# Performance work log

Measured on AMD Instinct MI355X. Metric: run time of the kernel, lower is better.

## Reference

```python
import jax, jax.numpy as jnp
import numpy as np

H = 56; W = 56; WS = 7; SHIFT = 3; HEADS = 4; DIM = 128
N = WS * WS  # 49 tokens per window
EPS = 1e-5


def _rel_pos_index():
    c = np.stack(np.meshgrid(np.arange(WS), np.arange(WS), indexing='ij')).reshape(2, -1)
    r = (c[:, :, None] - c[:, None, :]).transpose(1, 2, 0)
    r[..., 0] += WS - 1
    r[..., 1] += WS - 1
    r[..., 0] *= 2 * WS - 1
    return jnp.asarray(r.sum(-1))  # [N, N] int


def _attn_mask():
    img = np.zeros((H, W))
    sl = (slice(0, -WS), slice(-WS, -SHIFT), slice(-SHIFT, None))
    cnt = 0
    for hs in sl:
        for ws_ in sl:
            img[hs, ws_] = cnt
            cnt += 1
    mw = img.reshape(H // WS, WS, W // WS, WS).transpose(0, 2, 1, 3).reshape(-1, N)
    d = mw[:, None, :] - mw[:, :, None]  # [nW, N, N]
    return jnp.asarray(np.where(d != 0, -100.0, 0.0).astype(np.float32))


def _ln(x, w, b):
    m = x.mean(-1, keepdims=True)
    v = ((x - m) ** 2).mean(-1, keepdims=True)
    return (x - m) / jnp.sqrt(v + EPS) * w + b


def setup_inputs() -> dict:
    key = jax.random.key(0)
    ks = jax.random.split(key, 8)
    B = 64
    return {
        'x': jax.random.normal(ks[0], (B, H * W, DIM), jnp.float32),
        'qkv_w': jax.random.normal(ks[1], (DIM, 3 * DIM), jnp.float32) * 0.02,
        'qkv_b': jnp.zeros((3 * DIM,), jnp.float32),
        'proj_w': jax.random.normal(ks[2], (DIM, DIM), jnp.float32) * 0.02,
        'proj_b': jnp.zeros((DIM,), jnp.float32),
        'rpb_table': jax.random.normal(ks[3], ((2 * WS - 1) ** 2, HEADS), jnp.float32) * 0.02,
        'norm1_w': jnp.ones((DIM,), jnp.float32),
        'norm1_b': jnp.zeros((DIM,), jnp.float32),
        'norm2_w': jnp.ones((DIM,), jnp.float32),
        'norm2_b': jnp.zeros((DIM,), jnp.float32),
        'mlp_w1': jax.random.normal(ks[4], (DIM, 4 * DIM), jnp.float32) * 0.02,
        'mlp_b1': jnp.zeros((4 * DIM,), jnp.float32),
        'mlp_w2': jax.random.normal(ks[5], (4 * DIM, DIM), jnp.float32) * 0.02,
        'mlp_b2': jnp.zeros((DIM,), jnp.float32),
    }


def reference(x, qkv_w, qkv_b, proj_w, proj_b, rpb_table,
              norm1_w, norm1_b, norm2_w, norm2_b,
              mlp_w1, mlp_b1, mlp_w2, mlp_b2):
    B = x.shape[0]
    C = DIM
    hd = C // HEADS
    shortcut = x
    h = _ln(x, norm1_w, norm1_b).reshape(B, H, W, C)
    # cyclic shift
    h = jnp.roll(h, (-SHIFT, -SHIFT), axis=(1, 2))
    # window partition -> [B*nW, N, C]
    xw = h.reshape(B, H // WS, WS, W // WS, WS, C).transpose(0, 1, 3, 2, 4, 5).reshape(-1, N, C)
    qkv = (xw @ qkv_w + qkv_b).reshape(-1, N, 3, HEADS, hd).transpose(2, 0, 3, 1, 4)
    q, k, v = qkv[0] * (hd ** -0.5), qkv[1], qkv[2]  # [B*nW, heads, N, hd]
    attn = jnp.einsum('whnd,whmd->whnm', q, k)
    bias = rpb_table[_rel_pos_index().reshape(-1)].reshape(N, N, HEADS).transpose(2, 0, 1)
    attn = attn + bias[None]
    mask = _attn_mask()  # [nW, N, N]
    nW = mask.shape[0]
    attn = attn.reshape(B, nW, HEADS, N, N) + mask[None, :, None]
    attn = jax.nn.softmax(attn.reshape(-1, HEADS, N, N), axis=-1)
    out = jnp.einsum('whnm,whmd->wnhd', attn, v).reshape(-1, N, C)
    out = out @ proj_w + proj_b
    # window reverse + reverse shift
    out = out.reshape(B, H // WS, W // WS, WS, WS, C).transpose(0, 1, 3, 2, 4, 5).reshape(B, H, W, C)
    out = jnp.roll(out, (SHIFT, SHIFT), axis=(1, 2)).reshape(B, H * W, C)
    x = shortcut + out
    h2 = _ln(x, norm2_w, norm2_b)
    h2 = jax.nn.gelu(h2 @ mlp_w1 + mlp_b1, approximate=False) @ mlp_w2 + mlp_b2
    return x + h2
```

## Files before the change

### kernel.cpp

```cpp
#include <hip/hip_runtime.h>

#define HH 56
#define WW2 56
#define WS 7
#define SHIFT 3
#define HEADS 4
#define DIM 128
#define NTOK 49
#define BATCH 64
#define TOKENS (BATCH*HH*WW2)
#define NWIN 64
#define WINDOWS (BATCH*NWIN)

typedef __bf16 bf16x8 __attribute__((ext_vector_type(8)));
typedef float  f32x4  __attribute__((ext_vector_type(4)));

__device__ __forceinline__ unsigned short f2bf(float f) {
  unsigned u = __float_as_uint(f);
  u += 0x7fffu + ((u >> 16) & 1u);
  return (unsigned short)(u >> 16);
}

__device__ __forceinline__ void st4(unsigned short* p, float a, float b, float c, float d) {
  ushort4 pk; pk.x = f2bf(a); pk.y = f2bf(b); pk.z = f2bf(c); pk.w = f2bf(d);
  *(ushort4*)p = pk;
}

__device__ __forceinline__ int reg3(int g) { return g >= 53 ? 2 : (g >= 49 ? 1 : 0); }

__global__ __launch_bounds__(256) void k_prep(
    const float* __restrict__ qkv_w, const float* __restrict__ proj_w,
    const float* __restrict__ w1, const float* __restrict__ w2,
    unsigned short* __restrict__ qkvwT, unsigned short* __restrict__ projwT,
    unsigned short* __restrict__ w1T, unsigned short* __restrict__ w2T)
{
  int idx = blockIdx.x * 256 + threadIdx.x;
  if (idx < 49152) {
    int n = idx >> 7, k = idx & 127;
    qkvwT[idx] = f2bf(qkv_w[k * 384 + n]);
  } else if (idx < 65536) {
    int i = idx - 49152; int n = i >> 7, k = i & 127;
    projwT[i] = f2bf(proj_w[k * 128 + n]);
  } else if (idx < 131072) {
    int i = idx - 65536; int n = i >> 7, k = i & 127;
    w1T[i] = f2bf(w1[k * 512 + n]);
  } else {
    int i = idx - 131072; int n = i >> 9, k = i & 511;
    w2T[i] = f2bf(w2[k * 128 + n]);
  }
}

__global__ __launch_bounds__(256) void k_tbl(const float* __restrict__ rpb, float* __restrict__ tbl)
{
  int idx = blockIdx.x * 256 + threadIdx.x;
  int kt = idx & 63, qt = (idx >> 6) & 63, h = (idx >> 12) & 3, cls = idx >> 14;
  float v;
  if (qt >= NTOK || kt >= NTOK) v = -3e38f;
  else {
    int qi = qt / 7, qj = qt % 7, ki = kt / 7, kj = kt % 7;
    int bi = (cls & 2) ? 49 : 0, bj = (cls & 1) ? 49 : 0;
    int rq = reg3(bi + qi) * 3 + reg3(bj + qj);
    int rk = reg3(bi + ki) * 3 + reg3(bj + kj);
    v = rpb[((qi - ki + 6) * 13 + (qj - kj + 6)) * HEADS + h] + (rq != rk ? -100.0f : 0.0f);
  }
  tbl[idx] = v;
}

__global__ __launch_bounds__(256) void k_ln1_window(
    const float* __restrict__ x, const float* __restrict__ w,
    const float* __restrict__ b, unsigned short* __restrict__ xw)
{
  int lane = threadIdx.x & 63;
  int t = blockIdx.x * 4 + (threadIdx.x >> 6);
  const float* xp = x + (size_t)t * DIM;
  float2 v = *(const float2*)(xp + lane * 2);
  float s = v.x + v.y;
  float sq = v.x * v.x + v.y * v.y;
  #pragma unroll
  for (int off = 32; off; off >>= 1) {
    s += __shfl_xor(s, off);
    sq += __shfl_xor(sq, off);
  }
  float mean = s * (1.0f / DIM);
  float var = sq * (1.0f / DIM) - mean * mean;
  float rs = rsqrtf(var + 1e-5f);
  float2 wv = *(const float2*)(w + lane * 2);
  float2 bv = *(const float2*)(b + lane * 2);
  float y0 = (v.x - mean) * rs * wv.x + bv.x;
  float y1 = (v.y - mean) * rs * wv.y + bv.y;
  int bi = t / (HH * WW2);
  int r = t % (HH * WW2);
  int i = r / WW2, j = r % WW2;
  int si = i >= SHIFT ? i - SHIFT : i + (HH - SHIFT);
  int sj = j >= SHIFT ? j - SHIFT : j + (WW2 - SHIFT);
  int win = bi * NWIN + (si / WS) * 8 + (sj / WS);
  int tok = (si % WS) * WS + (sj % WS);
  unsigned pack = ((unsigned)f2bf(y1) << 16) | (unsigned)f2bf(y0);
  *(unsigned*)(xw + ((size_t)(win * NTOK + tok)) * DIM + lane * 2) = pack;
}

__global__ __launch_bounds__(256, 2) void k_attn(
    const unsigned short* __restrict__ xw,
    const unsigned short* __restrict__ qkvwT,
    const float* __restrict__ qkv_b,
    const unsigned short* __restrict__ projwT,
    const float* __restrict__ proj_b,
    const float* __restrict__ tbl,
    unsigned short* __restrict__ attn_out)
{
  __shared__ __align__(16) unsigned short s_x[64 * 136];
  __shared__ __align__(16) unsigned short s_qk[64 * 264];
  __shared__ __align__(16) unsigned short s_vT[128 * 72];

  int tid = threadIdx.x;
  int wave = tid >> 6;
  int lane = tid & 63;
  int l = lane & 15, g = lane >> 4;
  int win = blockIdx.x;
  int wi = (win & 63) >> 3, wj = win & 7;

  const unsigned short* xwin = xw + (size_t)win * (NTOK * DIM);
  for (int idx = tid; idx < NTOK * 16; idx += 256) {
    int row = idx >> 4, seg = idx & 15;
    *(uint4*)&s_x[row * 136 + seg * 8] = *(const uint4*)(xwin + row * DIM + seg * 8);
  }
  for (int idx = tid; idx < 15 * 17; idx += 256) {
    int row = 49 + idx / 17, seg = idx % 17;
    *(uint4*)&s_x[row * 136 + seg * 8] = make_uint4(0, 0, 0, 0);
  }
  __syncthreads();

  bf16x8 xf[4][4];
  #pragma unroll
  for (int nt = 0; nt < 4; ++nt)
    #pragma unroll
    for (int kk = 0; kk < 4; ++kk)
      xf[nt][kk] = *(const bf16x8*)&s_x[(nt * 16 + l) * 136 + kk * 32 + g * 8];

  #pragma unroll
  for (int wti = 0; wti < 6; ++wti) {
    int wt = wave * 6 + wti;
    bf16x8 wf[4];
    #pragma unroll
    for (int kk = 0; kk < 4; ++kk)
      wf[kk] = *(const bf16x8*)(qkvwT + (size_t)(wt * 16 + l) * DIM + kk * 32 + g * 8);
    f32x4 acc[4];
    #pragma unroll
    for (int nt = 0; nt < 4; ++nt) acc[nt] = (f32x4){0.f, 0.f, 0.f, 0.f};
    #pragma unroll
    for (int kk = 0; kk < 4; ++kk)
      #pragma unroll
      for (int nt = 0; nt < 4; ++nt)
        acc[nt] = __builtin_amdgcn_mfma_f32_16x16x32_bf16(wf[kk], xf[nt][kk], acc[nt], 0, 0, 0);
    float4 b4 = *(const float4*)(qkv_b + wt * 16 + g * 4);
    if (wt < 16) {
      float sc = wt < 8 ? 0.17677669529663687f : 1.0f;
      #pragma unroll
      for (int nt = 0; nt < 4; ++nt)
        st4(&s_qk[(nt * 16 + l) * 264 + wt * 16 + g * 4],
            (acc[nt][0] + b4.x) * sc, (acc[nt][1] + b4.y) * sc,
            (acc[nt][2] + b4.z) * sc, (acc[nt][3] + b4.w) * sc);
    } else {
      int d0 = wt * 16 - 256 + g * 4;
      #pragma unroll
      for (int nt = 0; nt < 4; ++nt) {
        s_vT[(d0 + 0) * 72 + nt * 16 + l] = f2bf(acc[nt][0] + b4.x);
        s_vT[(d0 + 1) * 72 + nt * 16 + l] = f2bf(acc[nt][1] + b4.y);
        s_vT[(d0 + 2) * 72 + nt * 16 + l] = f2bf(acc[nt][2] + b4.z);
        s_vT[(d0 + 3) * 72 + nt * 16 + l] = f2bf(acc[nt][3] + b4.w);
      }
    }
  }
  __syncthreads();

  int h = wave;
  bf16x8 kf[4], qf[4];
  #pragma unroll
  for (int mt = 0; mt < 4; ++mt)
    kf[mt] = *(const bf16x8*)&s_qk[(mt * 16 + l) * 264 + 128 + h * 32 + g * 8];
  #pragma unroll
  for (int nt = 0; nt < 4; ++nt)
    qf[nt] = *(const bf16x8*)&s_qk[(nt * 16 + l) * 264 + h * 32 + g * 8];
  __syncthreads();

  int clsid = ((wi == 7) ? 2 : 0) | ((wj == 7) ? 1 : 0);
  const float* tb = tbl + ((clsid * 4 + h) << 12);
  f32x4 sc[4][4];
  #pragma unroll
  for (int nt = 0; nt < 4; ++nt)
    #pragma unroll
    for (int mt = 0; mt < 4; ++mt) {
      f32x4 ci = *(const f32x4*)(tb + (nt * 16 + l) * 64 + mt * 16 + g * 4);
      sc[mt][nt] = __builtin_amdgcn_mfma_f32_16x16x32_bf16(kf[mt], qf[nt], ci, 0, 0, 0);
    }

  #pragma unroll
  for (int nt = 0; nt < 4; ++nt) {
    float m = sc[0][nt][0];
    #pragma unroll
    for (int mt = 0; mt < 4; ++mt)
      #pragma unroll
      for (int rr = 0; rr < 4; ++rr) m = fmaxf(m, sc[mt][nt][rr]);
    m = fmaxf(m, __shfl_xor(m, 16));
    m = fmaxf(m, __shfl_xor(m, 32));
    float ssum = 0.f;
    #pragma unroll
    for (int mt = 0; mt < 4; ++mt)
      #pragma unroll
      for (int rr = 0; rr < 4; ++rr) {
        float e = __expf(sc[mt][nt][rr] - m);
        sc[mt][nt][rr] = e;
        ssum += e;
      }
    ssum += __shfl_xor(ssum, 16);
    ssum += __shfl_xor(ssum, 32);
    float inv = 1.0f / ssum;
    #pragma unroll
    for (int mt = 0; mt < 4; ++mt)
      st4(&s_qk[(nt * 16 + l) * 264 + h * 64 + mt * 16 + g * 4],
          sc[mt][nt][0] * inv, sc[mt][nt][1] * inv, sc[mt][nt][2] * inv, sc[mt][nt][3] * inv);
  }

  bf16x8 vf[2][2], pf[4][2];
  #pragma unroll
  for (int dt = 0; dt < 2; ++dt)
    #pragma unroll
    for (int kk = 0; kk < 2; ++kk)
      vf[dt][kk] = *(const bf16x8*)&s_vT[(h * 32 + dt * 16 + l) * 72 + kk * 32 + g * 8];
  #pragma unroll
  for (int nt = 0; nt < 4; ++nt)
    #pragma unroll
    for (int kk = 0; kk < 2; ++kk)
      pf[nt][kk] = *(const bf16x8*)&s_qk[(nt * 16 + l) * 264 + h * 64 + kk * 32 + g * 8];
  #pragma unroll
  for (int dt = 0; dt < 2; ++dt)
    #pragma unroll
    for (int nt = 0; nt < 4; ++nt) {
      f32x4 a = (f32x4){0.f, 0.f, 0.f, 0.f};
      a = __builtin_amdgcn_mfma_f32_16x16x32_bf16(vf[dt][0], pf[nt][0], a, 0, 0, 0);
      a = __builtin_amdgcn_mfma_f32_16x16x32_bf16(vf[dt][1], pf[nt][1], a, 0, 0, 0);
      st4(&s_x[(nt * 16 + l) * 136 + h * 32 + dt * 16 + g * 4], a[0], a[1], a[2], a[3]);
    }
  __syncthreads();

  unsigned short* stage = s_vT;
  bf16x8 of[4][4];
  #pragma unroll
  for (int nt = 0; nt < 4; ++nt)
    #pragma unroll
    for (int kk = 0; kk < 4; ++kk)
      of[nt][kk] = *(const bf16x8*)&s_x[(nt * 16 + l) * 136 + kk * 32 + g * 8];
  #pragma unroll
  for (int wti = 0; wti < 2; ++wti) {
    int wt = wave * 2 + wti;
    bf16x8 wf[4];
    #pragma unroll
    for (int kk = 0; kk < 4; ++kk)
      wf[kk] = *(const bf16x8*)(projwT + (size_t)(wt * 16 + l) * DIM + kk * 32 + g * 8);
    f32x4 acc[4];
    #pragma unroll
    for (int nt = 0; nt < 4; ++nt) acc[nt] = (f32x4){0.f, 0.f, 0.f, 0.f};
    #pragma unroll
    for (int kk = 0; kk < 4; ++kk)
      #pragma unroll
      for (int nt = 0; nt < 4; ++nt)
        acc[nt] = __builtin_amdgcn_mfma_f32_16x16x32_bf16(wf[kk], of[nt][kk], acc[nt], 0, 0, 0);
    float4 b4 = *(const float4*)(proj_b + wt * 16 + g * 4);
    #pragma unroll
    for (int nt = 0; nt < 4; ++nt)
      st4(&stage[(nt * 16 + l) * 136 + wt * 16 + g * 4],
          acc[nt][0] + b4.x, acc[nt][1] + b4.y, acc[nt][2] + b4.z, acc[nt][3] + b4.w);
  }
  __syncthreads();

  unsigned short* outp = attn_out + (size_t)win * (NTOK * DIM);
  for (int idx = tid; idx < NTOK * 16; idx += 256) {
    int row = idx >> 4, seg = idx & 15;
    *(uint4*)(outp + idx * 8) = *(const uint4*)&stage[row * 136 + seg * 8];
  }
}

__device__ __forceinline__ float gelu_f(float x) {
  float x2 = x * x;
  float t = x * __builtin_fmaf(x2, -0.10294429f, -2.3022077f);
  float e = __builtin_amdgcn_exp2f(t);
  return x * __builtin_amdgcn_rcpf(1.0f + e);
}

__global__ __launch_bounds__(256) void k_mlp(
    const float* __restrict__ x, const unsigned short* __restrict__ attn,
    const float* __restrict__ n2w, const float* __restrict__ n2b,
    const unsigned short* __restrict__ w1T, const float* __restrict__ b1,
    const unsigned short* __restrict__ w2T, const float* __restrict__ b2,
    float* __restrict__ io)
{
  __shared__ __align__(16) unsigned short s_t[2][64 * 136];
  __shared__ float s_part[64][4][2];
  int tid = threadIdx.x;
  int wave = tid >> 6;
  int lane = tid & 63;
  int l = lane & 15, g = lane >> 4;
  size_t m0 = (size_t)blockIdx.x * 64;
  int col0 = wave * 32 + g * 4;

  float4 xz[4][2];
  float sA[4], sQ[4];
  #pragma unroll
  for (int nt = 0; nt < 4; ++nt) {
    int row = nt * 16 + l;
    int t = (int)m0 + row;
    int bi = t / (HH * WW2);
    int r = t % (HH * WW2);
    int i = r / WW2, j = r % WW2;
    int si = i >= SHIFT ? i - SHIFT : i + (HH - SHIFT);
    int sj = j >= SHIFT ? j - SHIFT : j + (WW2 - SHIFT);
    int win = bi * NWIN + (si / WS) * 8 + (sj / WS);
    int tok = (si % WS) * WS + (sj % WS);
    const float* xp = x + (size_t)t * DIM;
    const unsigned short* ap = attn + ((size_t)(win * NTOK + tok)) * DIM;
    float s = 0.f, sq = 0.f;
    #pragma unroll
    for (int wti = 0; wti < 2; ++wti) {
      int col = col0 + wti * 16;
      float4 xv = *(const float4*)(xp + col);
      ushort4 av = *(const ushort4*)(ap + col);
      float4 z;
      z.x = xv.x + __uint_as_float((unsigned)av.x << 16);
      z.y = xv.y + __uint_as_float((unsigned)av.y << 16);
      z.z = xv.z + __uint_as_float((unsigned)av.z << 16);
      z.w = xv.w + __uint_as_float((unsigned)av.w << 16);
      xz[nt][wti] = z;
      s += z.x + z.y + z.z + z.w;
      sq += z.x * z.x + z.y * z.y + z.z * z.z + z.w * z.w;
      *(float4*)(io + (size_t)t * DIM + col) = z;
    }
    s += __shfl_xor(s, 16); s += __shfl_xor(s, 32);
    sq += __shfl_xor(sq, 16); sq += __shfl_xor(sq, 32);
    sA[nt] = s; sQ[nt] = sq;
  }
  if (g == 0) {
    #pragma unroll
    for (int nt = 0; nt < 4; ++nt) {
      s_part[nt * 16 + l][wave][0] = sA[nt];
      s_part[nt * 16 + l][wave][1] = sQ[nt];
    }
  }
  __syncthreads();
  float4 wv0 = *(const float4*)(n2w + col0);
  float4 wv1 = *(const float4*)(n2w + col0 + 16);
  float4 bv0 = *(const float4*)(n2b + col0);
  float4 bv1 = *(const float4*)(n2b + col0 + 16);
  #pragma unroll
  for (int nt = 0; nt < 4; ++nt) {
    int row = nt * 16 + l;
    float s = 0.f, sq = 0.f;
    #pragma unroll
    for (int wv = 0; wv < 4; ++wv) { s += s_part[row][wv][0]; sq += s_part[row][wv][1]; }
    float mean = s * (1.0f / DIM);
    float var = sq * (1.0f / DIM) - mean * mean;
    float rs = rsqrtf(var + 1e-5f);
    float4 z0 = xz[nt][0], z1 = xz[nt][1];
    st4(&s_t[1][row * 136 + col0],
        (z0.x - mean) * rs * wv0.x + bv0.x, (z0.y - mean) * rs * wv0.y + bv0.y,
        (z0.z - mean) * rs * wv0.z + bv0.z, (z0.w - mean) * rs * wv0.w + bv0.w);
    st4(&s_t[1][row * 136 + col0 + 16],
        (z1.x - mean) * rs * wv1.x + bv1.x, (z1.y - mean) * rs * wv1.y + bv1.y,
        (z1.z - mean) * rs * wv1.z + bv1.z, (z1.w - mean) * rs * wv1.w + bv1.w);
  }
  __syncthreads();

  bf16x8 hf[4][4];
  #pragma unroll
  for (int nt = 0; nt < 4; ++nt)
    #pragma unroll
    for (int kk = 0; kk < 4; ++kk)
      hf[nt][kk] = *(const bf16x8*)&s_t[1][(nt * 16 + l) * 136 + kk * 32 + g * 8];

  f32x4 o[2][4];
  #pragma unroll
  for (int wti = 0; wti < 2; ++wti)
    #pragma unroll
    for (int nt = 0; nt < 4; ++nt) o[wti][nt] = (f32x4){0.f, 0.f, 0.f, 0.f};

  for (int c = 0; c < 4; ++c) {
    unsigned short* buf = s_t[c & 1];
    #pragma unroll
    for (int wti = 0; wti < 2; ++wti) {
      int wt = wave * 2 + wti;
      int n0 = c * 128 + wt * 16;
      bf16x8 wf[4];
      #pragma unroll
      for (int kk = 0; kk < 4; ++kk)
        wf[kk] = *(const bf16x8*)(w1T + (size_t)(n0 + l) * DIM + kk * 32 + g * 8);
      f32x4 acc[4];
      #pragma unroll
      for (int nt = 0; nt < 4; ++nt) acc[nt] = (f32x4){0.f, 0.f, 0.f, 0.f};
      #pragma unroll
      for (int kk = 0; kk < 4; ++kk)
        #pragma unroll
        for (int nt = 0; nt < 4; ++nt)
          acc[nt] = __builtin_amdgcn_mfma_f32_16x16x32_bf16(wf[kk], hf[nt][kk], acc[nt], 0, 0, 0);
      float4 b4 = *(const float4*)(b1 + n0 + g * 4);
      #pragma unroll
      for (int nt = 0; nt < 4; ++nt)
        st4(&buf[(nt * 16 + l) * 136 + wt * 16 + g * 4],
            gelu_f(acc[nt][0] + b4.x), gelu_f(acc[nt][1] + b4.y),
            gelu_f(acc[nt][2] + b4.z), gelu_f(acc[nt][3] + b4.w));
    }
    __syncthreads();
    #pragma unroll
    for (int kk = 0; kk < 4; ++kk) {
      bf16x8 tf[4];
      #pragma unroll
      for (int nt = 0; nt < 4; ++nt)
        tf[nt] = *(const bf16x8*)&buf[(nt * 16 + l) * 136 + kk * 32 + g * 8];
      #pragma unroll
      for (int wti = 0; wti < 2; ++wti) {
        int wt = wave * 2 + wti;
        bf16x8 wf2 = *(const bf16x8*)(w2T + (size_t)(wt * 16 + l) * 512 + c * 128 + kk * 32 + g * 8);
        #pragma unroll
        for (int nt = 0; nt < 4; ++nt)
          o[wti][nt] = __builtin_amdgcn_mfma_f32_16x16x32_bf16(wf2, tf[nt], o[wti][nt], 0, 0, 0);
      }
    }
  }

  #pragma unroll
  for (int wti = 0; wti < 2; ++wti) {
    int wt = wave * 2 + wti;
    float4 b4 = *(const float4*)(b2 + wt * 16 + g * 4);
    #pragma unroll
    for (int nt = 0; nt < 4; ++nt) {
      float* p = io + (m0 + nt * 16 + l) * DIM + wt * 16 + g * 4;
      float4 pv = *(float4*)p;
      pv.x += o[wti][nt][0] + b4.x;
      pv.y += o[wti][nt][1] + b4.y;
      pv.z += o[wti][nt][2] + b4.z;
      pv.w += o[wti][nt][3] + b4.w;
      *(float4*)p = pv;
    }
  }
}

extern "C" void kernel_launch(void* const* d_in, const int* in_sizes, int n_in,
                              void* d_out, int out_size, void* d_ws, size_t ws_size,
                              hipStream_t stream) {
  const float* x       = (const float*)d_in[0];
  const float* qkv_w   = (const float*)d_in[1];
  const float* qkv_b   = (const float*)d_in[2];
  const float* proj_w  = (const float*)d_in[3];
  const float* proj_b  = (const float*)d_in[4];
  const float* rpb     = (const float*)d_in[5];
  const float* n1w     = (const float*)d_in[6];
  const float* n1b     = (const float*)d_in[7];
  const float* n2w     = (const float*)d_in[8];
  const float* n2b     = (const float*)d_in[9];
  const float* mlp_w1  = (const float*)d_in[10];
  const float* mlp_b1  = (const float*)d_in[11];
  const float* mlp_w2  = (const float*)d_in[12];
  const float* mlp_b2  = (const float*)d_in[13];
  float* out = (float*)d_out;

  char* ws = (char*)d_ws;
  const size_t TOKB = (size_t)TOKENS * DIM * 2;
  unsigned short* xw     = (unsigned short*)(ws);
  unsigned short* attn_o = (unsigned short*)(ws + TOKB);
  unsigned short* qkvwT  = (unsigned short*)(ws + 2 * TOKB);
  unsigned short* projwT = (unsigned short*)(ws + 2 * TOKB + 98304);
  unsigned short* w1T    = (unsigned short*)(ws + 2 * TOKB + 98304 + 32768);
  unsigned short* w2T    = (unsigned short*)(ws + 2 * TOKB + 98304 + 32768 + 131072);
  float*          tbl    = (float*)(ws + 2 * TOKB + 98304 + 32768 + 131072 + 131072);

  k_prep<<<768, 256, 0, stream>>>(qkv_w, proj_w, mlp_w1, mlp_w2, qkvwT, projwT, w1T, w2T);
  k_tbl<<<256, 256, 0, stream>>>(rpb, tbl);
  k_ln1_window<<<TOKENS / 4, 256, 0, stream>>>(x, n1w, n1b, xw);
  k_attn<<<WINDOWS, 256, 0, stream>>>(xw, qkvwT, qkv_b, projwT, proj_b, tbl, attn_o);
  k_mlp<<<TOKENS / 64, 256, 0, stream>>>(x, attn_o, n2w, n2b, w1T, mlp_b1, w2T, mlp_b2, out);
}
```

Baseline: 500.2 us.

## Fuse LN1 and window partition into attention kernel; keep residual in registers

Removes the separate LN1/window-partition kernel: each attention block now gathers its shifted window rows directly from x in fp32, normalizes them and writes bf16 into shared memory. This removes a bf16 intermediate round trip through global memory and one launch. In the MLP kernel, the first residual sum is kept in registers and combined with the MLP output in a single store, instead of being written and then read back. The cost is more registers in the attention kernel, which holds 13 row pairs per lane, and strided gathers from x.

Result: faster. 465.9 us (-6.9%).

```diff
diff --git a/kernel.cpp b/kernel.cpp
--- a/kernel.cpp
+++ b/kernel.cpp
@@ -66,41 +66,9 @@
   tbl[idx] = v;
 }
 
-__global__ __launch_bounds__(256) void k_ln1_window(
-    const float* __restrict__ x, const float* __restrict__ w,
-    const float* __restrict__ b, unsigned short* __restrict__ xw)
-{
-  int lane = threadIdx.x & 63;
-  int t = blockIdx.x * 4 + (threadIdx.x >> 6);
-  const float* xp = x + (size_t)t * DIM;
-  float2 v = *(const float2*)(xp + lane * 2);
-  float s = v.x + v.y;
-  float sq = v.x * v.x + v.y * v.y;
-  #pragma unroll
-  for (int off = 32; off; off >>= 1) {
-    s += __shfl_xor(s, off);
-    sq += __shfl_xor(sq, off);
-  }
-  float mean = s * (1.0f / DIM);
-  float var = sq * (1.0f / DIM) - mean * mean;
-  float rs = rsqrtf(var + 1e-5f);
-  float2 wv = *(const float2*)(w + lane * 2);
-  float2 bv = *(const float2*)(b + lane * 2);
-  float y0 = (v.x - mean) * rs * wv.x + bv.x;
-  float y1 = (v.y - mean) * rs * wv.y + bv.y;
-  int bi = t / (HH * WW2);
-  int r = t % (HH * WW2);
-  int i = r / WW2, j = r % WW2;
-  int si = i >= SHIFT ? i - SHIFT : i + (HH - SHIFT);
-  int sj = j >= SHIFT ? j - SHIFT : j + (WW2 - SHIFT);
-  int win = bi * NWIN + (si / WS) * 8 + (sj / WS);
-  int tok = (si % WS) * WS + (sj % WS);
-  unsigned pack = ((unsigned)f2bf(y1) << 16) | (unsigned)f2bf(y0);
-  *(unsigned*)(xw + ((size_t)(win * NTOK + tok)) * DIM + lane * 2) = pack;
-}
-
 __global__ __launch_bounds__(256, 2) void k_attn(
-    const unsigned short* __restrict__ xw,
+    const float* __restrict__ x,
+    const float* __restrict__ n1w, const float* __restrict__ n1b,
     const unsigned short* __restrict__ qkvwT,
     const float* __restrict__ qkv_b,
     const unsigned short* __restrict__ projwT,
@@ -118,11 +86,43 @@
   int l = lane & 15, g = lane >> 4;
   int win = blockIdx.x;
   int wi = (win & 63) >> 3, wj = win & 7;
-
-  const unsigned short* xwin = xw + (size_t)win * (NTOK * DIM);
-  for (int idx = tid; idx < NTOK * 16; idx += 256) {
-    int row = idx >> 4, seg = idx & 15;
-    *(uint4*)&s_x[row * 136 + seg * 8] = *(const uint4*)(xwin + row * DIM + seg * 8);
+  int bi = win >> 6;
+
+  {
+    float2 wv1 = *(const float2*)(n1w + lane * 2);
+    float2 bv1 = *(const float2*)(n1b + lane * 2);
+    float2 vr[13];
+    #pragma unroll
+    for (int rr = 0; rr < 13; ++rr) {
+      int row = wave + rr * 4;
+      if (row < NTOK) {
+        int ti = row / 7, tj = row % 7;
+        int i = wi * WS + ti + SHIFT; if (i >= HH) i -= HH;
+        int j = wj * WS + tj + SHIFT; if (j >= WW2) j -= WW2;
+        const float* xp = x + ((size_t)(bi * (HH * WW2) + i * WW2 + j)) * DIM;
+        vr[rr] = *(const float2*)(xp + lane * 2);
+      }
+    }
+    #pragma unroll
+    for (int rr = 0; rr < 13; ++rr) {
+      int row = wave + rr * 4;
+      if (row < NTOK) {
+        float2 v = vr[rr];
+        float s = v.x + v.y, sq = v.x * v.x + v.y * v.y;
+        #pragma unroll
+        for (int off = 32; off; off >>= 1) {
+          s += __shfl_xor(s, off);
+          sq += __shfl_xor(sq, off);
+        }
+        float mean = s * (1.0f / DIM);
+        float var = sq * (1.0f / DIM) - mean * mean;
+        float rs = rsqrtf(var + 1e-5f);
+        float y0 = (v.x - mean) * rs * wv1.x + bv1.x;
+        float y1 = (v.y - mean) * rs * wv1.y + bv1.y;
+        unsigned pack = ((unsigned)f2bf(y1) << 16) | (unsigned)f2bf(y0);
+        *(unsigned*)&s_x[row * 136 + lane * 2] = pack;
+      }
+    }
   }
   for (int idx = tid; idx < 15 * 17; idx += 256) {
     int row = 49 + idx / 17, seg = idx % 17;
@@ -332,7 +332,6 @@
       xz[nt][wti] = z;
       s += z.x + z.y + z.z + z.w;
       sq += z.x * z.x + z.y * z.y + z.z * z.z + z.w * z.w;
-      *(float4*)(io + (size_t)t * DIM + col) = z;
     }
     s += __shfl_xor(s, 16); s += __shfl_xor(s, 32);
     sq += __shfl_xor(sq, 16); sq += __shfl_xor(sq, 32);
@@ -431,13 +430,13 @@
     float4 b4 = *(const float4*)(b2 + wt * 16 + g * 4);
     #pragma unroll
     for (int nt = 0; nt < 4; ++nt) {
-      float* p = io + (m0 + nt * 16 + l) * DIM + wt * 16 + g * 4;
-      float4 pv = *(float4*)p;
-      pv.x += o[wti][nt][0] + b4.x;
-      pv.y += o[wti][nt][1] + b4.y;
-      pv.z += o[wti][nt][2] + b4.z;
-      pv.w += o[wti][nt][3] + b4.w;
-      *(float4*)p = pv;
+      float4 z = xz[nt][wti];
+      float4 pv;
+      pv.x = z.x + o[wti][nt][0] + b4.x;
+      pv.y = z.y + o[wti][nt][1] + b4.y;
+      pv.z = z.z + o[wti][nt][2] + b4.z;
+      pv.w = z.w + o[wti][nt][3] + b4.w;
+      *(float4*)(io + (m0 + nt * 16 + l) * DIM + wt * 16 + g * 4) = pv;
     }
   }
 }
@@ -463,17 +462,15 @@
 
   char* ws = (char*)d_ws;
   const size_t TOKB = (size_t)TOKENS * DIM * 2;
-  unsigned short* xw     = (unsigned short*)(ws);
-  unsigned short* attn_o = (unsigned short*)(ws + TOKB);
-  unsigned short* qkvwT  = (unsigned short*)(ws + 2 * TOKB);
-  unsigned short* projwT = (unsigned short*)(ws + 2 * TOKB + 98304);
-  unsigned short* w1T    = (unsigned short*)(ws + 2 * TOKB + 98304 + 32768);
-  unsigned short* w2T    = (unsigned short*)(ws + 2 * TOKB + 98304 + 32768 + 131072);
-  float*          tbl    = (float*)(ws + 2 * TOKB + 98304 + 32768 + 131072 + 131072);
+  unsigned short* attn_o = (unsigned short*)(ws);
+  unsigned short* qkvwT  = (unsigned short*)(ws + TOKB);
+  unsigned short* projwT = (unsigned short*)(ws + TOKB + 98304);
+  unsigned short* w1T    = (unsigned short*)(ws + TOKB + 98304 + 32768);
+  unsigned short* w2T    = (unsigned short*)(ws + TOKB + 98304 + 32768 + 131072);
+  float*          tbl    = (float*)(ws + TOKB + 98304 + 32768 + 131072 + 131072);
 
   k_prep<<<768, 256, 0, stream>>>(qkv_w, proj_w, mlp_w1, mlp_w2, qkvwT, projwT, w1T, w2T);
   k_tbl<<<256, 256, 0, stream>>>(rpb, tbl);
-  k_ln1_window<<<TOKENS / 4, 256, 0, stream>>>(x, n1w, n1b, xw);
-  k_attn<<<WINDOWS, 256, 0, stream>>>(xw, qkvwT, qkv_b, projwT, proj_b, tbl, attn_o);
+  k_attn<<<WINDOWS, 256, 0, stream>>>(x, n1w, n1b, qkvwT, qkv_b, projwT, proj_b, tbl, attn_o);
   k_mlp<<<TOKENS / 64, 256, 0, stream>>>(x, attn_o, n2w, n2b, w1T, mlp_b1, w2T, mlp_b2, out);
 }
```
